# Optimization experiments

Measured on AMD Instinct MI355X. Metric: run time of the kernel, lower is better.

The kernel has to match this reference:

```python
import jax, jax.numpy as jnp
import numpy as np
from jax import lax

IN_DIM = 128
B, H, W = 4, 64, 64


def setup_inputs() -> dict:
    key = jax.random.key(0)
    ks = jax.random.split(key, 11)
    C = IN_DIM
    c8 = C // 8
    s = lambda k, shape, scale: jax.random.normal(k, shape, dtype=jnp.float32) * scale
    return {
        "x": s(ks[0], (B, C, H, W), 1.0),
        "x_forward": s(ks[1], (B, C, H, W), 1.0),
        "x_backward": s(ks[2], (B, C, H, W), 1.0),
        # 1x1 conv weights stored as [out, in]
        "Wq": s(ks[3], (c8, C), C ** -0.5),
        "bq": jnp.zeros((c8,), jnp.float32),
        "Wk": s(ks[4], (c8, C), C ** -0.5),
        "bk": jnp.zeros((c8,), jnp.float32),
        "Wv": s(ks[5], (C, C), C ** -0.5),
        "bv": jnp.zeros((C,), jnp.float32),
        # 3x3 conv weight [out=C, in=2C, kh, kw]
        "Wf": s(ks[6], (C, 2 * C, 3, 3), (2 * C * 9) ** -0.5),
        "bf": jnp.zeros((C,), jnp.float32),
    }


def _conv1x1(x, w, b):
    # x: [B,C,H,W], w: [O,C] -> [B,O,H,W]
    return jnp.einsum("bchw,oc->bohw", x, w) + b[None, :, None, None]


def reference(x, x_forward, x_backward, Wq, bq, Wk, bk, Wv, bv, Wf, bf):
    Bb, C, Hh, Ww = x.shape
    HW = Hh * Ww
    query = _conv1x1(x_forward, Wq, bq).reshape(Bb, -1, HW)   # [B,c8,HW]
    key = _conv1x1(x, Wk, bk).reshape(Bb, -1, HW)             # [B,c8,HW]
    value = _conv1x1(x_backward, Wv, bv).reshape(Bb, C, HW)   # [B,C,HW]

    # att_score[b, k_pos, q_pos] = key[b,:,k_pos] . query[b,:,q_pos]
    att_score = jnp.einsum("bck,bcq->bkq", key, query)        # [B,HW,HW]
    max_value = jnp.max(att_score, axis=-1)                   # [B,HW]
    idx = jnp.argmax(att_score, axis=-1)                      # [B,HW] int

    selected_value = jnp.take_along_axis(value, idx[:, None, :], axis=2)
    selected_value = selected_value.reshape(Bb, C, Hh, Ww)
    max_value = max_value.reshape(Bb, 1, Hh, Ww)

    front_res = jnp.concatenate([x, selected_value], axis=1)  # [B,2C,H,W]
    front_res = lax.conv_general_dilated(
        front_res, Wf, window_strides=(1, 1), padding="SAME",
        dimension_numbers=("NCHW", "OIHW", "NCHW"),
    ) + bf[None, :, None, None]
    front_res = front_res * max_value
    return x + front_res
```

## Files before the change

### kernel.cpp

```cpp
#include <hip/hip_runtime.h>

#define HW 4096
#define CC 128
#define MARGIN 2e-3f

typedef unsigned short ushort_t;
typedef unsigned int uint_t;
typedef __attribute__((ext_vector_type(8))) short short8;
typedef __attribute__((ext_vector_type(4))) float f32x4;

__device__ __forceinline__ float dot4(float4 a, float4 b) {
    return (a.x*b.x + a.y*b.y) + (a.z*b.z + a.w*b.w);
}

__device__ __forceinline__ ushort_t f2bf(float f) {
    union { float f; uint_t u; } cv; cv.f = f;
    uint_t r = cv.u + 0x7fffu + ((cv.u >> 16) & 1u);
    return (ushort_t)(r >> 16);
}

__device__ __forceinline__ float bf2f(ushort_t h) {
    union { uint_t u; float f; } cv; cv.u = ((uint_t)h) << 16;
    return cv.f;
}

__device__ __forceinline__ void store16(ushort_t* dst, const ushort_t* s) {
    union { ushort_t s[8]; uint4 v; } a, b;
    #pragma unroll
    for (int j = 0; j < 8; j++) { a.s[j] = s[j]; b.s[j] = s[8+j]; }
    *(uint4*)dst = a.v;
    *(uint4*)(dst + 8) = b.v;
}

__device__ __forceinline__ void gl2lds16(const ushort_t* g, ushort_t* l) {
    __builtin_amdgcn_global_load_lds(
        (const __attribute__((address_space(1))) unsigned int*)g,
        (__attribute__((address_space(3))) unsigned int*)l, 16, 0, 0);
}

__global__ __launch_bounds__(256) void prep_kernel(
    const float* __restrict__ x, const float* __restrict__ xf, const float* __restrict__ xb,
    const float* __restrict__ Wq, const float* __restrict__ bq,
    const float* __restrict__ Wk, const float* __restrict__ bk,
    const float* __restrict__ Wv, const float* __restrict__ bv,
    const float* __restrict__ Wf,
    float* __restrict__ Qt, float* __restrict__ Kt, float* __restrict__ V,
    ushort_t* __restrict__ Qs, ushort_t* __restrict__ KB,
    ushort_t* __restrict__ xsel, ushort_t* __restrict__ Wt)
{
    __shared__ __align__(16) unsigned char smem[16704];
    int bid = blockIdx.x;
    int tid = threadIdx.x;

    if (bid < 512) {
        bool isQ = bid < 256;
        int sub = bid & 255;
        int b = sub >> 6, pt = sub & 63;
        const float* src  = isQ ? xf : x;
        const float* W    = isQ ? Wq : Wk;
        const float* bias = isQ ? bq : bk;
        int ph = tid >> 6, pl = tid & 63;
        int p = pt*64 + pl;
        int pg = (b << 12) + p;
        const float* sp = src + ((size_t)b << 19) + p + ((size_t)(ph*32) << 12);

        float acc[16];
        #pragma unroll
        for (int o = 0; o < 16; o++) acc[o] = ph ? 0.f : bias[o];

        for (int cc = 0; cc < 32; cc += 4) {
            float x0 = sp[(size_t)(cc+0) << 12];
            float x1 = sp[(size_t)(cc+1) << 12];
            float x2 = sp[(size_t)(cc+2) << 12];
            float x3 = sp[(size_t)(cc+3) << 12];
            #pragma unroll
            for (int o = 0; o < 16; o++) {
                float4 w = *(const float4*)&W[o*128 + ph*32 + cc];
                acc[o] += w.x*x0 + w.y*x1 + w.z*x2 + w.w*x3;
            }
        }

        float* sAcc = (float*)smem;
        if (ph) {
            float* dst = sAcc + (ph-1)*1088 + pl*17;
            #pragma unroll
            for (int o = 0; o < 16; o++) dst[o] = acc[o];
        }
        __syncthreads();
        if (!ph) {
            const float* s0 = sAcc + pl*17;
            const float* s1 = sAcc + 1088 + pl*17;
            const float* s2 = sAcc + 2176 + pl*17;
            #pragma unroll
            for (int o = 0; o < 16; o++) acc[o] += s0[o] + s1[o] + s2[o];

            float* dstF = isQ ? Qt : Kt;
            float4* df = (float4*)(dstF + (size_t)pg * 16);
            df[0] = make_float4(acc[0],acc[1],acc[2],acc[3]);
            df[1] = make_float4(acc[4],acc[5],acc[6],acc[7]);
            df[2] = make_float4(acc[8],acc[9],acc[10],acc[11]);
            df[3] = make_float4(acc[12],acc[13],acc[14],acc[15]);

            ushort_t h[16], m[16], l[16];
            #pragma unroll
            for (int d = 0; d < 16; d++) {
                h[d] = f2bf(acc[d]);
                float r1 = acc[d] - bf2f(h[d]);
                m[d] = f2bf(r1);
                l[d] = f2bf(r1 - bf2f(m[d]));
            }
            if (isQ) {
                ushort_t* o_ = Qs + (size_t)pg*64;
                store16(o_,      h);
                store16(o_ + 16, m);
                store16(o_ + 32, h);
                store16(o_ + 48, l);
            } else {
                int u = b*256 + (p >> 4);
                int n = p & 15;
                ushort_t* o_ = KB + (size_t)u*1536 + n*32;
                store16(o_,        h); store16(o_ + 16,   h);
                store16(o_ + 512,  m); store16(o_ + 528,  m);
                store16(o_ + 1024, l); store16(o_ + 1040, h);
            }
        }
    } else if (bid < 1536) {
        int vbid = bid - 512;
        int b = vbid >> 8, og = (vbid >> 4) & 15, pt = vbid & 15;
        float* sW = (float*)smem;
        for (int e = tid; e < 1024; e += 256) sW[e] = Wv[og*1024 + e];
        __syncthreads();

        int p = pt*256 + tid;
        const float* sp = xb + ((size_t)b << 19) + p;

        float acc[8];
        #pragma unroll
        for (int j = 0; j < 8; j++) acc[j] = 0.f;

        for (int c4 = 0; c4 < 128; c4 += 4) {
            float x0 = sp[(size_t)(c4+0) << 12];
            float x1 = sp[(size_t)(c4+1) << 12];
            float x2 = sp[(size_t)(c4+2) << 12];
            float x3 = sp[(size_t)(c4+3) << 12];
            #pragma unroll
            for (int j = 0; j < 8; j++) {
                float4 w = *(const float4*)&sW[j*128 + c4];
                acc[j] += w.x*x0 + w.y*x1 + w.z*x2 + w.w*x3;
            }
        }
        float* vr = V + ((size_t)((b << 12) + p))*128 + og*8;
        float4 r0 = make_float4(acc[0]+bv[og*8+0], acc[1]+bv[og*8+1],
                                acc[2]+bv[og*8+2], acc[3]+bv[og*8+3]);
        float4 r1 = make_float4(acc[4]+bv[og*8+4], acc[5]+bv[og*8+5],
                                acc[6]+bv[og*8+6], acc[7]+bv[og*8+7]);
        *(float4*)vr = r0;
        *(float4*)(vr + 4) = r1;
    } else if (bid < 1792) {
        ushort_t* sT = (ushort_t*)smem;
        int xbid = bid - 1536;
        int b = xbid >> 6, y = xbid & 63;
        int cq = tid >> 6, xx = tid & 63;
        const float* src = x + ((size_t)b << 19) + (y << 6) + xx;
        #pragma unroll 4
        for (int k = 0; k < 32; k++) {
            int c = cq*32 + k;
            sT[xx*130 + c] = f2bf(src[(size_t)c << 12]);
        }
        __syncthreads();
        uint_t* dst = (uint_t*)(xsel + ((size_t)(b*4356 + (y+1)*66 + 1))*256);
        #pragma unroll
        for (int k = 0; k < 16; k++) {
            int idx = k*256 + tid;
            int s = idx >> 6, u = idx & 63;
            uint_t v = *(const uint_t*)&sT[s*130 + u*2];
            dst[s*128 + u] = v;
        }
    } else if (bid < 1922) {
        int g = (bid - 1792) * 256 + tid;
        if (g < 33280) {
            int b = g / 8320;
            int rem = g - b * 8320;
            int si = rem >> 5;
            int ch = rem & 31;
            int y, xx;
            if (si < 66)      { y = 0;  xx = si; }
            else if (si < 132){ y = 65; xx = si - 66; }
            else { int t = si - 132; y = 1 + (t >> 1); xx = (t & 1) ? 65 : 0; }
            int site = y * 66 + xx;
            uint4* dst = (uint4*)(xsel + ((size_t)(b*4356 + site))*256);
            dst[ch] = make_uint4(0,0,0,0);
        }
    } else {
        int t = (bid - 1922) * 256 + tid;
        if (t < 36864) {
            int cg = t & 3;
            int o = (t >> 2) & 31;
            int tc = t >> 7;
            int tap = tc % 9;
            int rest = tc / 9;
            int cb = rest & 7, og = rest >> 3;
            union { ushort_t s[8]; uint4 v; } pk;
            #pragma unroll
            for (int j = 0; j < 8; j++) {
                int ci = cg*8 + j;
                pk.s[j] = f2bf(Wf[(size_t)(og*32 + o)*2304 + (cb*32 + ci)*9 + tap]);
            }
            *(uint4*)(Wt + (size_t)t*8) = pk.v;
        }
    }
}

__global__ __launch_bounds__(512, 2) void att_kernel(
    const ushort_t* __restrict__ Qs, const ushort_t* __restrict__ KB,
    const float* __restrict__ Qt, const float* __restrict__ Kt,
    float* __restrict__ maxv, int* __restrict__ idxv)
{
    __shared__ float sM1[64*33];
    __shared__ int   sI1[64*33];
    __shared__ float sM2[64*33];
    __shared__ int sCnt;
    __shared__ int sList[64];

    int bid = blockIdx.x;
    int kg = bid & 63, b = bid >> 6;
    int tid = threadIdx.x;
    int wave = tid >> 6, lane = tid & 63;
    int l15 = lane & 15, quad = lane >> 4;

    short8 Bf[4][3];
    const ushort_t* kb = KB + ((size_t)((b*256 + kg*4)*3))*512 + l15*32 + quad*8;
    #pragma unroll
    for (int t = 0; t < 4; t++)
        #pragma unroll
        for (int p = 0; p < 3; p++)
            Bf[t][p] = *(const short8*)(kb + (size_t)(t*3 + p)*512);

    const ushort_t* qbase = Qs + ((size_t)(b*4096 + wave*512 + l15))*64 + quad*8;

    float m1[4], m2[4]; int i1[4];
    #pragma unroll
    for (int t = 0; t < 4; t++) { m1[t] = -1e30f; m2[t] = -1e30f; i1[t] = 0; }

    for (int it = 0; it < 32; it++) {
        const ushort_t* aptr = qbase + it*1024;
        short8 A1 = *(const short8*)aptr;
        short8 A2 = *(const short8*)(aptr + 32);
        f32x4 acc[4];
        #pragma unroll
        for (int t = 0; t < 4; t++) {
            acc[t] = (f32x4)0.f;
            acc[t] = __builtin_amdgcn_mfma_f32_16x16x32_bf16(A1, Bf[t][0], acc[t], 0, 0, 0);
            acc[t] = __builtin_amdgcn_mfma_f32_16x16x32_bf16(A1, Bf[t][1], acc[t], 0, 0, 0);
            acc[t] = __builtin_amdgcn_mfma_f32_16x16x32_bf16(A2, Bf[t][2], acc[t], 0, 0, 0);
        }
        int q0 = wave*512 + it*16 + quad*4;
        #pragma unroll
        for (int r = 0; r < 4; r++) {
            int cand = q0 + r;
            #pragma unroll
            for (int t = 0; t < 4; t++) {
                float d = acc[t][r];
                float old1 = m1[t];
                bool gt = d > old1;
                m1[t] = gt ? d : old1;
                i1[t] = gt ? cand : i1[t];
                m2[t] = __builtin_amdgcn_fmed3f(d, old1, m2[t]);
            }
        }
    }

    #pragma unroll
    for (int t = 0; t < 4; t++) {
        int kl_ = t*16 + l15;
        int slot = wave*4 + quad;
        sM1[kl_*33 + slot] = m1[t];
        sI1[kl_*33 + slot] = i1[t];
        sM2[kl_*33 + slot] = m2[t];
    }
    if (tid == 0) sCnt = 0;
    __syncthreads();
    if (tid < 64) {
        float M1 = -1e30f; int I1 = 0x7fffffff;
        for (int s = 0; s < 32; s++) {
            float m = sM1[tid*33 + s]; int i = sI1[tid*33 + s];
            if (m > M1 || (m == M1 && i < I1)) { M1 = m; I1 = i; }
        }
        float M2 = -1e30f;
        for (int s = 0; s < 32; s++) {
            float m = sM1[tid*33 + s]; int i = sI1[tid*33 + s];
            float cnd = (i == I1) ? sM2[tid*33 + s] : m;
            M2 = fmaxf(M2, cnd);
        }
        int row = (b << 12) + kg*64 + tid;
        maxv[row] = M1; idxv[row] = I1;
        if (M1 - M2 < MARGIN) {
            int s = atomicAdd(&sCnt, 1);
            sList[s] = tid;
        }
    }
    __syncthreads();

    int n = sCnt;
    float* sRm = sM1;
    int*   sRi = sI1;
    for (int e = 0; e < n; e++) {
        int local = sList[e];
        int row = (b << 12) + kg*64 + local;
        const float4* Kp = (const float4*)(Kt + (size_t)row*16);
        float4 ka = Kp[0], kb2 = Kp[1], kc = Kp[2], kd = Kp[3];
        const float4* Qp = (const float4*)(Qt + (((size_t)b) << 12)*16);
        float m = -1e30f; int i = 0;
        #pragma unroll
        for (int j = 0; j < 8; j++) {
            int q = tid*8 + j;
            float4 qa = Qp[q*4+0], qb = Qp[q*4+1], qc = Qp[q*4+2], qd = Qp[q*4+3];
            float d = (dot4(ka,qa) + dot4(kb2,qb)) + (dot4(kc,qc) + dot4(kd,qd));
            if (d > m) { m = d; i = q; }
        }
        sRm[tid] = m; sRi[tid] = i;
        __syncthreads();
        #pragma unroll
        for (int s = 256; s > 0; s >>= 1) {
            if (tid < s) {
                float mo = sRm[tid+s]; int io = sRi[tid+s];
                if (mo > sRm[tid] || (mo == sRm[tid] && io < sRi[tid])) {
                    sRm[tid] = mo; sRi[tid] = io;
                }
            }
            __syncthreads();
        }
        if (tid == 0) { maxv[row] = sRm[0]; idxv[row] = sRi[0]; }
        __syncthreads();
    }
}

__global__ __launch_bounds__(256) void gather_kernel(
    const float* __restrict__ V, const int* __restrict__ idxv,
    ushort_t* __restrict__ xsel)
{
    int bid = blockIdx.x;
    int b = bid >> 6, pt = bid & 63;
    int tid = threadIdx.x;
    int pp = tid >> 2, cq = tid & 3;
    int p = pt*64 + pp;
    int ip = idxv[(b << 12) + p];
    const float* vrow = V + ((size_t)((b << 12) + ip))*128 + cq*32;
    int site = ((p >> 6) + 1)*66 + (p & 63) + 1;
    ushort_t* dst = xsel + ((size_t)(b*4356 + site))*256 + 128 + cq*32;
    #pragma unroll
    for (int k = 0; k < 4; k++) {
        float4 a = *(const float4*)(vrow + k*8);
        float4 c = *(const float4*)(vrow + k*8 + 4);
        union { ushort_t s[8]; uint4 v; } pk;
        pk.s[0] = f2bf(a.x); pk.s[1] = f2bf(a.y); pk.s[2] = f2bf(a.z); pk.s[3] = f2bf(a.w);
        pk.s[4] = f2bf(c.x); pk.s[5] = f2bf(c.y); pk.s[6] = f2bf(c.z); pk.s[7] = f2bf(c.w);
        *(uint4*)(dst + k*8) = pk.v;
    }
}

__global__ __launch_bounds__(256) void conv_kernel(
    const float* __restrict__ x, const ushort_t* __restrict__ xsel,
    const ushort_t* __restrict__ Wt, const float* __restrict__ bf,
    const float* __restrict__ maxv, float* __restrict__ out)
{
    __shared__ __align__(16) ushort_t sIn[2][336*32];
    __shared__ __align__(16) ushort_t sW[2][9*32*32];

    int bid = blockIdx.x;
    int og = bid & 3, tx = (bid >> 2) & 3, ty = (bid >> 4) & 3, b = bid >> 6;
    int tid = threadIdx.x;
    int wave = tid >> 6, lane = tid & 63;
    int l15 = lane & 15, quad = lane >> 4;

    const ushort_t* xsel_base = xsel + ((size_t)(b*4356 + (ty*16)*66 + tx*16))*256;
    const ushort_t* wt_base   = Wt + (size_t)og*8*9216;

    f32x4 acc[4][2];
    #pragma unroll
    for (int mi = 0; mi < 4; mi++)
        #pragma unroll
        for (int ni = 0; ni < 2; ni++) acc[mi][ni] = (f32x4)0.f;

    int l4q = lane >> 2, l4 = lane & 3;

    for (int r = wave; r < 21; r += 4) {
        int site = r*16 + l4q;
        int iy = site / 18, ix = site - iy*18;
        const ushort_t* g = xsel_base + (size_t)(iy*66 + ix)*256 + l4*8;
        gl2lds16(g, &sIn[0][r*512]);
    }
    for (int r = wave; r < 18; r += 4) {
        const ushort_t* g = wt_base + r*512 + lane*8;
        gl2lds16(g, &sW[0][r*512]);
    }
    __syncthreads();

    for (int cb = 0; cb < 8; cb++) {
        int cur = cb & 1;
        if (cb < 7) {
            int nb = cur ^ 1;
            for (int r = wave; r < 21; r += 4) {
                int site = r*16 + l4q;
                int iy = site / 18, ix = site - iy*18;
                const ushort_t* g = xsel_base + (size_t)(iy*66 + ix)*256 + (cb+1)*32 + l4*8;
                gl2lds16(g, &sIn[nb][r*512]);
            }
            for (int r = wave; r < 18; r += 4) {
                const ushort_t* g = wt_base + (size_t)(cb+1)*9216 + r*512 + lane*8;
                gl2lds16(g, &sW[nb][r*512]);
            }
        }

        #pragma unroll
        for (int tap = 0; tap < 9; tap++) {
            const int dy = tap / 3, dx = tap % 3;
            short8 B0 = *(const short8*)&sW[cur][(tap*32 +      l15)*32 + quad*8];
            short8 B1 = *(const short8*)&sW[cur][(tap*32 + 16 + l15)*32 + quad*8];
            #pragma unroll
            for (int mi = 0; mi < 4; mi++) {
                int row = wave*4 + mi + dy;
                short8 A = *(const short8*)&sIn[cur][(row*18 + l15 + dx)*32 + quad*8];
                acc[mi][0] = __builtin_amdgcn_mfma_f32_16x16x32_bf16(A, B0, acc[mi][0], 0, 0, 0);
                acc[mi][1] = __builtin_amdgcn_mfma_f32_16x16x32_bf16(A, B1, acc[mi][1], 0, 0, 0);
            }
        }
        __syncthreads();
    }

    int y0 = ty*16, x0 = tx*16;
    const float* xb_ = x   + ((size_t)b << 19);
    float*       ob  = out + ((size_t)b << 19);
    const float* mxb = maxv + (b << 12);
    #pragma unroll
    for (int mi = 0; mi < 4; mi++) {
        int y = y0 + wave*4 + mi;
        int p = (y << 6) + x0 + quad*4;
        float4 mv = *(const float4*)&mxb[p];
        #pragma unroll
        for (int ni = 0; ni < 2; ni++) {
            int o = og*32 + ni*16 + l15;
            float bfo = bf[o];
            float4 xv = *(const float4*)&xb_[((size_t)o << 12) + p];
            float4 r;
            r.x = xv.x + mv.x * (acc[mi][ni][0] + bfo);
            r.y = xv.y + mv.y * (acc[mi][ni][1] + bfo);
            r.z = xv.z + mv.z * (acc[mi][ni][2] + bfo);
            r.w = xv.w + mv.w * (acc[mi][ni][3] + bfo);
            *(float4*)&ob[((size_t)o << 12) + p] = r;
        }
    }
}

extern "C" void kernel_launch(void* const* d_in, const int* in_sizes, int n_in,
                              void* d_out, int out_size, void* d_ws, size_t ws_size,
                              hipStream_t stream) {
    (void)in_sizes; (void)n_in; (void)out_size; (void)ws_size;
    const float* x  = (const float*)d_in[0];
    const float* xf = (const float*)d_in[1];
    const float* xb = (const float*)d_in[2];
    const float* Wq = (const float*)d_in[3];
    const float* bq = (const float*)d_in[4];
    const float* Wk = (const float*)d_in[5];
    const float* bk = (const float*)d_in[6];
    const float* Wv = (const float*)d_in[7];
    const float* bv = (const float*)d_in[8];
    const float* Wf = (const float*)d_in[9];
    const float* bf = (const float*)d_in[10];
    float* out = (float*)d_out;

    float* ws   = (float*)d_ws;
    float* Qt   = ws;
    float* Kt   = Qt + 262144;
    float* V    = Kt + 262144;
    float* mx   = V  + 2097152;
    int*   idxv = (int*)(mx + 16384);
    ushort_t* Qs   = (ushort_t*)(idxv + 16384);
    ushort_t* KB   = Qs + 1048576;
    ushort_t* xsel = KB + 1572864;
    ushort_t* Wt   = xsel + 4460544;

    hipLaunchKernelGGL(prep_kernel,   dim3(2066), dim3(256), 0, stream,
                       x, xf, xb, Wq, bq, Wk, bk, Wv, bv, Wf,
                       Qt, Kt, V, Qs, KB, xsel, Wt);
    hipLaunchKernelGGL(att_kernel,    dim3(256), dim3(512), 0, stream,
                       Qs, KB, Qt, Kt, mx, idxv);
    hipLaunchKernelGGL(gather_kernel, dim3(256), dim3(256), 0, stream, V, idxv, xsel);
    hipLaunchKernelGGL(conv_kernel,   dim3(256), dim3(256), 0, stream, x, xsel, Wt, bf, mx, out);
}
```

Before: 171.9 us.

## Fuse value gather into attention kernel, store V as bf16, reuse conv A fragments

V is now written as bf16 in the prep kernel, which halves its footprint. The separate gather kernel is removed: the attention kernel keeps the argmax indices in shared memory and copies the selected bf16 value rows straight into the padded xsel buffer. This drops one launch, the global idx round trip, and the fp32 V reads. The conv inner loop is also reordered by dx so six A fragments are loaded once and reused across the three dy taps, which cuts LDS reads at the cost of more registers.

Result: no change. 173.9 us (+1.1%).

```diff
diff --git a/kernel.cpp b/kernel.cpp
--- a/kernel.cpp
+++ b/kernel.cpp
@@ -44,7 +44,7 @@
     const float* __restrict__ Wk, const float* __restrict__ bk,
     const float* __restrict__ Wv, const float* __restrict__ bv,
     const float* __restrict__ Wf,
-    float* __restrict__ Qt, float* __restrict__ Kt, float* __restrict__ V,
+    float* __restrict__ Qt, float* __restrict__ Kt, ushort_t* __restrict__ V,
     ushort_t* __restrict__ Qs, ushort_t* __restrict__ KB,
     ushort_t* __restrict__ xsel, ushort_t* __restrict__ Wt)
 {
@@ -149,13 +149,10 @@
                 acc[j] += w.x*x0 + w.y*x1 + w.z*x2 + w.w*x3;
             }
         }
-        float* vr = V + ((size_t)((b << 12) + p))*128 + og*8;
-        float4 r0 = make_float4(acc[0]+bv[og*8+0], acc[1]+bv[og*8+1],
-                                acc[2]+bv[og*8+2], acc[3]+bv[og*8+3]);
-        float4 r1 = make_float4(acc[4]+bv[og*8+4], acc[5]+bv[og*8+5],
-                                acc[6]+bv[og*8+6], acc[7]+bv[og*8+7]);
-        *(float4*)vr = r0;
-        *(float4*)(vr + 4) = r1;
+        union { ushort_t s[8]; uint4 u; } pk;
+        #pragma unroll
+        for (int j = 0; j < 8; j++) pk.s[j] = f2bf(acc[j] + bv[og*8 + j]);
+        *(uint4*)(V + ((size_t)((b << 12) + p))*128 + og*8) = pk.u;
     } else if (bid < 1792) {
         ushort_t* sT = (ushort_t*)smem;
         int xbid = bid - 1536;
@@ -214,13 +211,15 @@
 __global__ __launch_bounds__(512, 2) void att_kernel(
     const ushort_t* __restrict__ Qs, const ushort_t* __restrict__ KB,
     const float* __restrict__ Qt, const float* __restrict__ Kt,
-    float* __restrict__ maxv, int* __restrict__ idxv)
+    const ushort_t* __restrict__ V, float* __restrict__ maxv,
+    ushort_t* __restrict__ xsel)
 {
     __shared__ float sM1[64*33];
     __shared__ int   sI1[64*33];
     __shared__ float sM2[64*33];
     __shared__ int sCnt;
     __shared__ int sList[64];
+    __shared__ int sIdx[64];
 
     int bid = blockIdx.x;
     int kg = bid & 63, b = bid >> 6;
@@ -293,7 +292,8 @@
             M2 = fmaxf(M2, cnd);
         }
         int row = (b << 12) + kg*64 + tid;
-        maxv[row] = M1; idxv[row] = I1;
+        maxv[row] = M1;
+        sIdx[tid] = I1;
         if (M1 - M2 < MARGIN) {
             int s = atomicAdd(&sCnt, 1);
             sList[s] = tid;
@@ -330,32 +330,21 @@
             }
             __syncthreads();
         }
-        if (tid == 0) { maxv[row] = sRm[0]; idxv[row] = sRi[0]; }
-        __syncthreads();
-    }
-}
-
-__global__ __launch_bounds__(256) void gather_kernel(
-    const float* __restrict__ V, const int* __restrict__ idxv,
-    ushort_t* __restrict__ xsel)
-{
-    int bid = blockIdx.x;
-    int b = bid >> 6, pt = bid & 63;
-    int tid = threadIdx.x;
-    int pp = tid >> 2, cq = tid & 3;
-    int p = pt*64 + pp;
-    int ip = idxv[(b << 12) + p];
-    const float* vrow = V + ((size_t)((b << 12) + ip))*128 + cq*32;
-    int site = ((p >> 6) + 1)*66 + (p & 63) + 1;
-    ushort_t* dst = xsel + ((size_t)(b*4356 + site))*256 + 128 + cq*32;
-    #pragma unroll
-    for (int k = 0; k < 4; k++) {
-        float4 a = *(const float4*)(vrow + k*8);
-        float4 c = *(const float4*)(vrow + k*8 + 4);
-        union { ushort_t s[8]; uint4 v; } pk;
-        pk.s[0] = f2bf(a.x); pk.s[1] = f2bf(a.y); pk.s[2] = f2bf(a.z); pk.s[3] = f2bf(a.w);
-        pk.s[4] = f2bf(c.x); pk.s[5] = f2bf(c.y); pk.s[6] = f2bf(c.z); pk.s[7] = f2bf(c.w);
-        *(uint4*)(dst + k*8) = pk.v;
+        if (tid == 0) { maxv[row] = sRm[0]; sIdx[local] = sRi[0]; }
+        __syncthreads();
+    }
+
+    const ushort_t* Vb = V + (((size_t)b) << 12)*128;
+    #pragma unroll
+    for (int rd = 0; rd < 2; rd++) {
+        int j = rd*32 + (tid >> 4);
+        int lane16 = tid & 15;
+        int p = kg*64 + j;
+        int ip = sIdx[j];
+        const uint4* src = (const uint4*)(Vb + (size_t)ip*128 + lane16*8);
+        int site = ((p >> 6) + 1)*66 + (p & 63) + 1;
+        uint4* dst = (uint4*)(xsel + ((size_t)(b*4356 + site))*256 + 128 + lane16*8);
+        *dst = *src;
     }
 }
 
@@ -413,16 +402,21 @@
         }
 
         #pragma unroll
-        for (int tap = 0; tap < 9; tap++) {
-            const int dy = tap / 3, dx = tap % 3;
-            short8 B0 = *(const short8*)&sW[cur][(tap*32 +      l15)*32 + quad*8];
-            short8 B1 = *(const short8*)&sW[cur][(tap*32 + 16 + l15)*32 + quad*8];
-            #pragma unroll
-            for (int mi = 0; mi < 4; mi++) {
-                int row = wave*4 + mi + dy;
-                short8 A = *(const short8*)&sIn[cur][(row*18 + l15 + dx)*32 + quad*8];
-                acc[mi][0] = __builtin_amdgcn_mfma_f32_16x16x32_bf16(A, B0, acc[mi][0], 0, 0, 0);
-                acc[mi][1] = __builtin_amdgcn_mfma_f32_16x16x32_bf16(A, B1, acc[mi][1], 0, 0, 0);
+        for (int dx = 0; dx < 3; dx++) {
+            short8 Ar[6];
+            #pragma unroll
+            for (int r = 0; r < 6; r++)
+                Ar[r] = *(const short8*)&sIn[cur][((wave*4 + r)*18 + l15 + dx)*32 + quad*8];
+            #pragma unroll
+            for (int dy = 0; dy < 3; dy++) {
+                int tap = dy*3 + dx;
+                short8 B0 = *(const short8*)&sW[cur][(tap*32 +      l15)*32 + quad*8];
+                short8 B1 = *(const short8*)&sW[cur][(tap*32 + 16 + l15)*32 + quad*8];
+                #pragma unroll
+                for (int mi = 0; mi < 4; mi++) {
+                    acc[mi][0] = __builtin_amdgcn_mfma_f32_16x16x32_bf16(Ar[mi+dy], B0, acc[mi][0], 0, 0, 0);
+                    acc[mi][1] = __builtin_amdgcn_mfma_f32_16x16x32_bf16(Ar[mi+dy], B1, acc[mi][1], 0, 0, 0);
+                }
             }
         }
         __syncthreads();
@@ -472,10 +466,9 @@
     float* ws   = (float*)d_ws;
     float* Qt   = ws;
     float* Kt   = Qt + 262144;
-    float* V    = Kt + 262144;
-    float* mx   = V  + 2097152;
-    int*   idxv = (int*)(mx + 16384);
-    ushort_t* Qs   = (ushort_t*)(idxv + 16384);
+    ushort_t* V = (ushort_t*)(Kt + 262144);
+    float* mx   = (float*)(V + 2097152);
+    ushort_t* Qs   = (ushort_t*)(mx + 16384);
     ushort_t* KB   = Qs + 1048576;
     ushort_t* xsel = KB + 1572864;
     ushort_t* Wt   = xsel + 4460544;
@@ -484,7 +477,7 @@
                        x, xf, xb, Wq, bq, Wk, bk, Wv, bv, Wf,
                        Qt, Kt, V, Qs, KB, xsel, Wt);
     hipLaunchKernelGGL(att_kernel,    dim3(256), dim3(512), 0, stream,
-                       Qs, KB, Qt, Kt, mx, idxv);
-    hipLaunchKernelGGL(gather_kernel, dim3(256), dim3(256), 0, stream, V, idxv, xsel);
-    hipLaunchKernelGGL(conv_kernel,   dim3(256), dim3(256), 0, stream, x, xsel, Wt, bf, mx, out);
-}
+                       Qs, KB, Qt, Kt, V, mx, xsel);
+    hipLaunchKernelGGL(conv_kernel,   dim3(256), dim3(256), 0, stream,
+                       x, xsel, Wt, bf, mx, out);
+}
```
